# Optimization experiments

Hardware: AMD Instinct MI355X
Metric: run time of the kernel (lower is better)

The kernel has to match this reference:

```python
import jax, jax.numpy as jnp
import numpy as np

B, L, D, H = 2, 2048, 2048, 16
C = D // H  # head dim = 128
EPS = 1e-5


def setup_inputs() -> dict:
    key = jax.random.key(0)
    k1, k2, k3, k4 = jax.random.split(key, 4)
    scale = 1.0 / np.sqrt(D)
    return {
        "x": jax.random.normal(k1, (B, L, D), dtype=jnp.float32),
        "theta": jax.random.uniform(k2, (B, L, D // 2), dtype=jnp.float32) * 6.2831853,
        "w_qkv": jax.random.normal(k3, (3 * D, D), dtype=jnp.float32) * scale,
        "w_y": jax.random.normal(k4, (D, D), dtype=jnp.float32) * scale,
        "b_y": jnp.zeros((D,), dtype=jnp.float32),
    }


def _rms_norm(t):
    # RMSNorm over last dim, eps=1e-5, no affine
    return t * jax.lax.rsqrt(jnp.mean(t * t, axis=-1, keepdims=True) + EPS)


def _apply_rope(q, k, theta):
    # q, k: (B, H, L, C); theta: (B, H, L, C//2)
    qr, qi = q[..., 0::2], q[..., 1::2]
    kr, ki = k[..., 0::2], k[..., 1::2]
    cos_t, sin_t = jnp.cos(theta), jnp.sin(theta)
    q_rot = jnp.stack((qr * cos_t - qi * sin_t, qr * sin_t + qi * cos_t), axis=-1).reshape(q.shape)
    k_rot = jnp.stack((kr * cos_t - ki * sin_t, kr * sin_t + ki * cos_t), axis=-1).reshape(k.shape)
    return q_rot, k_rot


def reference(x, theta, w_qkv, w_y, b_y):
    # QKV projection: (B, L, 3D)
    qkv = jnp.einsum("bld,ed->ble", x, w_qkv)
    # rearrange '... L (n H C) -> n ... H L C'
    qkv = qkv.reshape(B, L, 3, H, C).transpose(2, 0, 3, 1, 4)  # (3, B, H, L, C)
    q, k, v = qkv[0], qkv[1], qkv[2]
    q, k = _rms_norm(q), _rms_norm(k)
    # theta: (B, L, H*C/2) -> (B, H, L, C/2)
    th = theta.reshape(B, L, H, C // 2).transpose(0, 2, 1, 3)
    q, k = _apply_rope(q, k, th)
    # scaled dot-product attention
    scores = jnp.einsum("bhqc,bhkc->bhqk", q, k) / np.sqrt(C).astype(np.float32)
    attn = jax.nn.softmax(scores, axis=-1)
    y = jnp.einsum("bhqk,bhkc->bhqc", attn, v)
    # (B, H, L, C) -> (B, L, H*C)
    y = y.transpose(0, 2, 1, 3).reshape(B, L, D)
    return jnp.einsum("bld,ed->ble", y, w_y) + b_y
```

## Files before the change

kernel.cpp:

```cpp
#include <hip/hip_runtime.h>
#include <stdint.h>

typedef uint16_t u16;
typedef __attribute__((ext_vector_type(8))) short bf16x8;
typedef __attribute__((ext_vector_type(4))) float f32x4;


__device__ __forceinline__ u16 f2bf(float f) {
  uint32_t u = __builtin_bit_cast(uint32_t, f);
  u += 0x7fffu + ((u >> 16) & 1u);
  return (u16)(u >> 16);
}
__device__ __forceinline__ float bf2f(u16 h) {
  return __builtin_bit_cast(float, (uint32_t)h << 16);
}
__device__ __forceinline__ uint32_t pack2bf(float a, float b) {
  uint32_t ua = __builtin_bit_cast(uint32_t, a) + 0x7fffu;
  uint32_t ub = __builtin_bit_cast(uint32_t, b) + 0x7fffu;
  return (ua >> 16) | (ub & 0xffff0000u);
}
__device__ __forceinline__ void gl_lds16(const u16* g, u16* l) {
  __builtin_amdgcn_global_load_lds((const __attribute__((address_space(1))) uint32_t*)g,
                                   (__attribute__((address_space(3))) uint32_t*)l, 16, 0, 0);
}

__global__ __launch_bounds__(256) void castk(const float* __restrict__ in,
                                             u16* __restrict__ out, int n) {
  int idx = (blockIdx.x * 256 + threadIdx.x) * 4;
  int stride = gridDim.x * 256 * 4;
  for (int i = idx; i < n; i += stride) {
    float4 v = *(const float4*)(in + i);
    uint32_t lo = (uint32_t)f2bf(v.x) | ((uint32_t)f2bf(v.y) << 16);
    uint32_t hi = (uint32_t)f2bf(v.z) | ((uint32_t)f2bf(v.w) << 16);
    *(uint2*)(out + i) = make_uint2(lo, hi);
  }
}

template <int MODE>
__global__ __launch_bounds__(256) void gemm_nt(
    const u16* __restrict__ A, const u16* __restrict__ Bw, int K,
    u16* __restrict__ qb, u16* __restrict__ kb, u16* __restrict__ vt,
    float* __restrict__ out, const float* __restrict__ bias) {
  __shared__ u16 As[128 * 64];
  __shared__ u16 Bs[128 * 64];
  const int tid = threadIdx.x;
  const int lane = tid & 63, wid = tid >> 6;
  const int g = lane >> 4, lr = lane & 15;
  const int wm = wid >> 1, wn = wid & 1;
  const int m0 = blockIdx.y * 128, n0 = blockIdx.x * 128;
  f32x4 acc[4][4] = {};
  const int nk = K >> 6;
  for (int kt = 0; kt < nk; ++kt) {
    const int kbase = kt * 64;
#pragma unroll
    for (int i = 0; i < 4; ++i) {
      int ci = wid * 256 + i * 64 + lane;
      int row = ci >> 3, j = ci & 7;
      int js = j ^ (row & 7);
      gl_lds16(A + (size_t)(m0 + row) * K + kbase + js * 8, &As[(wid * 256 + i * 64) * 8]);
    }
#pragma unroll
    for (int i = 0; i < 4; ++i) {
      int ci = wid * 256 + i * 64 + lane;
      int row = ci >> 3, j = ci & 7;
      int js = j ^ (row & 7);
      gl_lds16(Bw + (size_t)(n0 + row) * K + kbase + js * 8, &Bs[(wid * 256 + i * 64) * 8]);
    }
    __syncthreads();
#pragma unroll
    for (int ks = 0; ks < 2; ++ks) {
      bf16x8 af[4], bfr[4];
#pragma unroll
      for (int t = 0; t < 4; ++t) {
        int ra = wm * 64 + t * 16 + lr;
        af[t] = *(const bf16x8*)&As[ra * 64 + (((ks * 4 + g) ^ (ra & 7)) * 8)];
        int rb = wn * 64 + t * 16 + lr;
        bfr[t] = *(const bf16x8*)&Bs[rb * 64 + (((ks * 4 + g) ^ (rb & 7)) * 8)];
      }
#pragma unroll
      for (int mt = 0; mt < 4; ++mt)
#pragma unroll
        for (int nt = 0; nt < 4; ++nt)
          acc[mt][nt] =
              __builtin_amdgcn_mfma_f32_16x16x32_bf16(af[mt], bfr[nt], acc[mt][nt], 0, 0, 0);
    }
    __syncthreads();
  }
  if (MODE == 0) {
    const int s = n0 >> 11;
    const int h = (n0 >> 7) & 15;
#pragma unroll
    for (int mt = 0; mt < 4; ++mt)
#pragma unroll
      for (int nt = 0; nt < 4; ++nt) {
        int cblk = wn * 64 + nt * 16 + lr;
#pragma unroll
        for (int r = 0; r < 4; ++r) {
          int m = m0 + wm * 64 + mt * 16 + g * 4 + r;
          int b = m >> 11, lpos = m & 2047;
          u16 val = f2bf(acc[mt][nt][r]);
          if (s < 2) {
            u16* dst = (s == 0) ? qb : kb;
            dst[(size_t)((b * 16 + h) * 2048 + lpos) * 128 + cblk] = val;
          } else {
            vt[(size_t)((b * 16 + h) * 128 + cblk) * 2048 + lpos] = val;
          }
        }
      }
  } else {
#pragma unroll
    for (int mt = 0; mt < 4; ++mt)
#pragma unroll
      for (int nt = 0; nt < 4; ++nt) {
        int n = n0 + wn * 64 + nt * 16 + lr;
        float bv = bias[n];
#pragma unroll
        for (int r = 0; r < 4; ++r) {
          int m = m0 + wm * 64 + mt * 16 + g * 4 + r;
          out[(size_t)m * 2048 + n] = acc[mt][nt][r] + bv;
        }
      }
  }
}

__global__ __launch_bounds__(256) void qk_fix(u16* __restrict__ qb, u16* __restrict__ kb,
                                              const float* __restrict__ theta) {
  const int row = blockIdx.x * 4 + (threadIdx.x >> 6);
  const int lane = threadIdx.x & 63;
  const int bh = row >> 11, l = row & 2047;
  const int b = bh >> 4, h = bh & 15;
  float th = theta[(size_t)(b * 2048 + l) * 1024 + h * 64 + lane];
  float sn, cs;
  __sincosf(th, &sn, &cs);
#pragma unroll
  for (int which = 0; which < 2; ++which) {
    u16* buf = which ? kb : qb;
    uint32_t* p = (uint32_t*)(buf + (size_t)row * 128) + lane;
    uint32_t v = *p;
    float x0 = bf2f((u16)(v & 0xffff)), x1 = bf2f((u16)(v >> 16));
    float ss = x0 * x0 + x1 * x1;
#pragma unroll
    for (int m = 1; m <= 32; m <<= 1) ss += __shfl_xor(ss, m);
    float rn = rsqrtf(ss * (1.0f / 128.0f) + 1e-5f);
    if (which == 0) rn *= 0.12751743f;
    x0 *= rn;
    x1 *= rn;
    float y0 = x0 * cs - x1 * sn;
    float y1 = x0 * sn + x1 * cs;
    *p = (uint32_t)f2bf(y0) | ((uint32_t)f2bf(y1) << 16);
  }
}

__global__ __launch_bounds__(256, 2) void attn_k(const u16* __restrict__ qb,
                                                 const u16* __restrict__ kb,
                                                 const u16* __restrict__ vt,
                                                 u16* __restrict__ yb) {
  __shared__ u16 sm[32768];
  const int gid = blockIdx.x;
  const int slot = gid & 7, rest = gid >> 3;
  const int bh = slot * 4 + (rest & 3);
  const int qtile = rest >> 2;
  const int b = bh >> 4, h = bh & 15;
  const int tid = threadIdx.x, lane = tid & 63, wid = tid >> 6;
  const int g = lane >> 4, lr = lane & 15;
  const int q0 = qtile * 128 + wid * 32;

  bf16x8 qf[2][4];
#pragma unroll
  for (int qs = 0; qs < 2; ++qs) {
    const u16* qrow = qb + (size_t)(bh * 2048 + q0 + qs * 16 + lr) * 128;
#pragma unroll
    for (int ks = 0; ks < 4; ++ks) qf[qs][ks] = *(const bf16x8*)&qrow[ks * 32 + g * 8];
  }

  auto stage = [&](int buf, int kv) {
#pragma unroll
    for (int i = 0; i < 4; ++i) {
      int ci = i * 256 + tid;
      int row = ci >> 4, j = ci & 15;
      gl_lds16(kb + (size_t)(bh * 2048 + kv + row) * 128 + (j ^ (row & 7)) * 8,
               &sm[buf * 8192 + ci * 8]);
    }
#pragma unroll
    for (int i = 0; i < 4; ++i) {
      int ci = i * 256 + tid;
      int row = ci >> 3, j = ci & 7;
      gl_lds16(vt + (size_t)(bh * 128 + row) * 2048 + kv + (j ^ (row & 7)) * 8,
               &sm[16384 + buf * 8192 + ci * 8]);
    }
  };

  f32x4 acc[2][8] = {};
  float mrun[2] = {-1e30f, -1e30f}, lrun[2] = {0.f, 0.f};
  const int sA = (2 * (g & 1)) * 16 + lr, sB = sA + 16;
  const bool hi2 = (g >> 1) != 0;

  stage(0, 0);
  asm volatile("s_waitcnt vmcnt(0)" ::: "memory");
  __builtin_amdgcn_s_barrier();

  for (int t = 0; t < 32; ++t) {
    const int cur = t & 1;
    if (t < 31) stage(cur ^ 1, (t + 1) * 64);
    const u16* Ks = &sm[cur * 8192];
    const u16* Vs = &sm[16384 + cur * 8192];

    f32x4 st[2][4] = {};
#pragma unroll
    for (int ks = 0; ks < 4; ++ks) {
      bf16x8 kf[4];
#pragma unroll
      for (int kt = 0; kt < 4; ++kt) {
        int row = kt * 16 + lr;
        kf[kt] = *(const bf16x8*)&Ks[row * 128 + (((ks * 4 + g) ^ (row & 7)) * 8)];
      }
#pragma unroll
      for (int kt = 0; kt < 4; ++kt)
#pragma unroll
        for (int qs = 0; qs < 2; ++qs)
          st[qs][kt] =
              __builtin_amdgcn_mfma_f32_16x16x32_bf16(kf[kt], qf[qs][ks], st[qs][kt], 0, 0, 0);
    }

    float pmax[2];
#pragma unroll
    for (int qs = 0; qs < 2; ++qs) {
      float mx = st[qs][0][0];
#pragma unroll
      for (int kt = 0; kt < 4; ++kt)
#pragma unroll
        for (int r = 0; r < 4; ++r) mx = fmaxf(mx, st[qs][kt][r]);
      mx = fmaxf(mx, __shfl_xor(mx, 16));
      mx = fmaxf(mx, __shfl_xor(mx, 32));
      pmax[qs] = mx;
    }
    float need = fmaxf(pmax[0] - mrun[0], pmax[1] - mrun[1]);
    if (!__all(need <= 8.0f)) {
#pragma unroll
      for (int qs = 0; qs < 2; ++qs) {
        float mnew = fmaxf(mrun[qs], pmax[qs]);
        float corr = __builtin_amdgcn_exp2f(mrun[qs] - mnew);
        lrun[qs] *= corr;
        mrun[qs] = mnew;
#pragma unroll
        for (int ct = 0; ct < 8; ++ct) {
          acc[qs][ct][0] *= corr;
          acc[qs][ct][1] *= corr;
          acc[qs][ct][2] *= corr;
          acc[qs][ct][3] *= corr;
        }
      }
    }
    uint32_t pw[2][4][2];
#pragma unroll
    for (int qs = 0; qs < 2; ++qs) {
      float rsum = 0.f;
#pragma unroll
      for (int kt = 0; kt < 4; ++kt)
#pragma unroll
        for (int hf = 0; hf < 2; ++hf) {
          float e0 = __builtin_amdgcn_exp2f(st[qs][kt][2 * hf] - mrun[qs]);
          float e1 = __builtin_amdgcn_exp2f(st[qs][kt][2 * hf + 1] - mrun[qs]);
          rsum += e0 + e1;
          pw[qs][kt][hf] = pack2bf(e0, e1);
        }
      rsum += __shfl_xor(rsum, 16);
      rsum += __shfl_xor(rsum, 32);
      lrun[qs] += rsum;
    }

#pragma unroll
    for (int ks2 = 0; ks2 < 2; ++ks2) {
      bf16x8 pf[2];
#pragma unroll
      for (int qs = 0; qs < 2; ++qs) {
        uint32_t a0 = __shfl(pw[qs][ks2 * 2][0], sA);
        uint32_t a1 = __shfl(pw[qs][ks2 * 2][1], sA);
        uint32_t a2 = __shfl(pw[qs][ks2 * 2][0], sB);
        uint32_t a3 = __shfl(pw[qs][ks2 * 2][1], sB);
        uint32_t b0 = __shfl(pw[qs][ks2 * 2 + 1][0], sA);
        uint32_t b1 = __shfl(pw[qs][ks2 * 2 + 1][1], sA);
        uint32_t b2 = __shfl(pw[qs][ks2 * 2 + 1][0], sB);
        uint32_t b3 = __shfl(pw[qs][ks2 * 2 + 1][1], sB);
        union {
          uint32_t u[4];
          bf16x8 v;
        } tt;
        tt.u[0] = hi2 ? b0 : a0;
        tt.u[1] = hi2 ? b1 : a1;
        tt.u[2] = hi2 ? b2 : a2;
        tt.u[3] = hi2 ? b3 : a3;
        pf[qs] = tt.v;
      }
#pragma unroll
      for (int ct = 0; ct < 8; ++ct) {
        int row = ct * 16 + lr;
        bf16x8 vf = *(const bf16x8*)&Vs[row * 64 + (((ks2 * 4 + g) ^ (row & 7)) * 8)];
#pragma unroll
        for (int qs = 0; qs < 2; ++qs)
          acc[qs][ct] = __builtin_amdgcn_mfma_f32_16x16x32_bf16(vf, pf[qs], acc[qs][ct], 0, 0, 0);
      }
    }
    if (t < 31) {
      asm volatile("s_waitcnt vmcnt(0)" ::: "memory");
      __builtin_amdgcn_s_barrier();
    }
  }

#pragma unroll
  for (int qs = 0; qs < 2; ++qs) {
    float inv = 1.f / lrun[qs];
    const size_t orow = (size_t)(b * 2048 + q0 + qs * 16 + lr) * 2048 + h * 128;
#pragma unroll
    for (int ct = 0; ct < 8; ++ct) {
      uint32_t lo = pack2bf(acc[qs][ct][0] * inv, acc[qs][ct][1] * inv);
      uint32_t hi = pack2bf(acc[qs][ct][2] * inv, acc[qs][ct][3] * inv);
      *(uint2*)&yb[orow + ct * 16 + g * 4] = make_uint2(lo, hi);
    }
  }
}

extern "C" void kernel_launch(void* const* d_in, const int* in_sizes, int n_in,
                              void* d_out, int out_size, void* d_ws, size_t ws_size,
                              hipStream_t stream) {
  const float* x = (const float*)d_in[0];
  const float* theta = (const float*)d_in[1];
  const float* wqkv = (const float*)d_in[2];
  const float* wy = (const float*)d_in[3];
  const float* by = (const float*)d_in[4];
  float* out = (float*)d_out;
  char* ws = (char*)d_ws;
  u16* xb  = (u16*)(ws + 0);
  u16* wqb = (u16*)(ws + 16777216);
  u16* wyb = (u16*)(ws + 41943040);
  u16* qb  = (u16*)(ws + 50331648);
  u16* kb  = (u16*)(ws + 67108864);
  u16* vt  = (u16*)(ws + 83886080);
  u16* yb  = (u16*)(ws + 100663296);

  castk<<<2048, 256, 0, stream>>>(x, xb, 2 * 2048 * 2048);
  castk<<<2048, 256, 0, stream>>>(wqkv, wqb, 3 * 2048 * 2048);
  castk<<<1024, 256, 0, stream>>>(wy, wyb, 2048 * 2048);

  gemm_nt<0><<<dim3(48, 32), 256, 0, stream>>>(xb, wqb, 2048, qb, kb, vt, nullptr, nullptr);
  qk_fix<<<16384, 256, 0, stream>>>(qb, kb, theta);
  attn_k<<<512, 256, 0, stream>>>(qb, kb, vt, yb);
  gemm_nt<1><<<dim3(16, 32), 256, 0, stream>>>(yb, wyb, 2048, nullptr, nullptr, nullptr, out, by);
}
```

Baseline: 306.2 us.

## Replace QKV GEMM with 256x256-tile 8-wave double-buffered pipelined kernel

```diff
diff --git a/kernel.cpp b/kernel.cpp
--- a/kernel.cpp
+++ b/kernel.cpp
@@ -36,10 +36,112 @@
   }
 }
 
-template <int MODE>
-__global__ __launch_bounds__(256) void gemm_nt(
+__global__ __launch_bounds__(512, 2) void gemm8_qkv(
+    const u16* __restrict__ A, const u16* __restrict__ Bw,
+    u16* __restrict__ qb, u16* __restrict__ kb, u16* __restrict__ vt) {
+  __shared__ u16 sm[65536];
+  const int K = 2048;
+  const int tid = threadIdx.x, lane = tid & 63;
+  const int wid = tid >> 6, g = lane >> 4, lr = lane & 15;
+  const int wm = wid >> 2, wn = wid & 3;
+  const int m0 = blockIdx.y * 256, n0 = blockIdx.x * 256;
+  const int x7 = lr & 7;
+  const int srow = tid >> 3, sj = tid & 7, sjs = sj ^ (srow & 7);
+
+  auto stA = [&](int buf, int kt, int R) {
+    gl_lds16(A + (size_t)(m0 + R + srow) * K + kt * 64 + sjs * 8,
+             &sm[buf * 32768 + R * 64 + tid * 8]);
+  };
+  auto stB = [&](int buf, int kt, int R) {
+    gl_lds16(Bw + (size_t)(n0 + R + srow) * K + kt * 64 + sjs * 8,
+             &sm[buf * 32768 + 16384 + R * 64 + tid * 8]);
+  };
+
+  f32x4 acc[8][4] = {};
+
+  stB(0, 0, 0); stB(0, 0, 64); stB(0, 0, 128); stB(0, 0, 192);
+  stA(0, 0, 0); stA(0, 0, 128); stA(0, 0, 64); stA(0, 0, 192);
+  asm volatile("s_waitcnt vmcnt(2)" ::: "memory");
+  __builtin_amdgcn_s_barrier();
+
+  for (int t = 0; t < 32; ++t) {
+    const int cur = t & 1, nxt = cur ^ 1;
+    const int kn = (t < 31) ? t + 1 : 31;
+    const u16* As = &sm[cur * 32768];
+    const u16* Bs = &sm[cur * 32768 + 16384];
+    bf16x8 bfr[4][2];
+#pragma unroll
+    for (int p = 0; p < 4; ++p) {
+      bf16x8 af[2][2];
+#pragma unroll
+      for (int i = 0; i < 2; ++i)
+#pragma unroll
+        for (int ks = 0; ks < 2; ++ks)
+          af[i][ks] = *(const bf16x8*)&As[(wm * 128 + (p * 2 + i) * 16 + lr) * 64 +
+                                          (((ks * 4 + g) ^ x7) * 8)];
+      if (p == 0) {
+#pragma unroll
+        for (int nf = 0; nf < 4; ++nf)
+#pragma unroll
+          for (int ks = 0; ks < 2; ++ks)
+            bfr[nf][ks] = *(const bf16x8*)&Bs[(wn * 64 + nf * 16 + lr) * 64 +
+                                              (((ks * 4 + g) ^ x7) * 8)];
+        stB(nxt, kn, 0);
+        stB(nxt, kn, 64);
+      } else if (p == 1) {
+        stB(nxt, kn, 128);
+        stB(nxt, kn, 192);
+      } else if (p == 2) {
+        stA(nxt, kn, 0);
+        stA(nxt, kn, 128);
+      } else {
+        stA(nxt, kn, 64);
+        stA(nxt, kn, 192);
+      }
+      __builtin_amdgcn_s_barrier();
+      asm volatile("s_waitcnt lgkmcnt(0)" ::: "memory");
+      __builtin_amdgcn_sched_barrier(0);
+      __builtin_amdgcn_s_setprio(1);
+#pragma unroll
+      for (int i = 0; i < 2; ++i)
+#pragma unroll
+        for (int nf = 0; nf < 4; ++nf) {
+          acc[p * 2 + i][nf] = __builtin_amdgcn_mfma_f32_16x16x32_bf16(
+              af[i][0], bfr[nf][0], acc[p * 2 + i][nf], 0, 0, 0);
+          acc[p * 2 + i][nf] = __builtin_amdgcn_mfma_f32_16x16x32_bf16(
+              af[i][1], bfr[nf][1], acc[p * 2 + i][nf], 0, 0, 0);
+        }
+      __builtin_amdgcn_s_setprio(0);
+      if (p == 1) asm volatile("s_waitcnt vmcnt(4)" ::: "memory");
+      if (p == 3) asm volatile("s_waitcnt vmcnt(2)" ::: "memory");
+      __builtin_amdgcn_s_barrier();
+    }
+  }
+
+  const int s = n0 >> 11;
+#pragma unroll
+  for (int mf = 0; mf < 8; ++mf)
+#pragma unroll
+    for (int nf = 0; nf < 4; ++nf) {
+      int n = n0 + wn * 64 + nf * 16 + lr;
+      int h = (n >> 7) & 15, cb = n & 127;
+#pragma unroll
+      for (int r = 0; r < 4; ++r) {
+        int m = m0 + wm * 128 + mf * 16 + g * 4 + r;
+        int b = m >> 11, lp = m & 2047;
+        u16 val = f2bf(acc[mf][nf][r]);
+        if (s == 0)
+          qb[(size_t)((b * 16 + h) * 2048 + lp) * 128 + cb] = val;
+        else if (s == 1)
+          kb[(size_t)((b * 16 + h) * 2048 + lp) * 128 + cb] = val;
+        else
+          vt[(size_t)((b * 16 + h) * 128 + cb) * 2048 + lp] = val;
+      }
+    }
+}
+
+__global__ __launch_bounds__(256) void gemm_out(
     const u16* __restrict__ A, const u16* __restrict__ Bw, int K,
-    u16* __restrict__ qb, u16* __restrict__ kb, u16* __restrict__ vt,
     float* __restrict__ out, const float* __restrict__ bias) {
   __shared__ u16 As[128 * 64];
   __shared__ u16 Bs[128 * 64];
@@ -86,41 +188,18 @@
     }
     __syncthreads();
   }
-  if (MODE == 0) {
-    const int s = n0 >> 11;
-    const int h = (n0 >> 7) & 15;
-#pragma unroll
-    for (int mt = 0; mt < 4; ++mt)
-#pragma unroll
-      for (int nt = 0; nt < 4; ++nt) {
-        int cblk = wn * 64 + nt * 16 + lr;
-#pragma unroll
-        for (int r = 0; r < 4; ++r) {
-          int m = m0 + wm * 64 + mt * 16 + g * 4 + r;
-          int b = m >> 11, lpos = m & 2047;
-          u16 val = f2bf(acc[mt][nt][r]);
-          if (s < 2) {
-            u16* dst = (s == 0) ? qb : kb;
-            dst[(size_t)((b * 16 + h) * 2048 + lpos) * 128 + cblk] = val;
-          } else {
-            vt[(size_t)((b * 16 + h) * 128 + cblk) * 2048 + lpos] = val;
-          }
-        }
-      }
-  } else {
-#pragma unroll
-    for (int mt = 0; mt < 4; ++mt)
-#pragma unroll
-      for (int nt = 0; nt < 4; ++nt) {
-        int n = n0 + wn * 64 + nt * 16 + lr;
-        float bv = bias[n];
-#pragma unroll
-        for (int r = 0; r < 4; ++r) {
-          int m = m0 + wm * 64 + mt * 16 + g * 4 + r;
-          out[(size_t)m * 2048 + n] = acc[mt][nt][r] + bv;
-        }
-      }
-  }
+#pragma unroll
+  for (int mt = 0; mt < 4; ++mt)
+#pragma unroll
+    for (int nt = 0; nt < 4; ++nt) {
+      int n = n0 + wn * 64 + nt * 16 + lr;
+      float bv = bias[n];
+#pragma unroll
+      for (int r = 0; r < 4; ++r) {
+        int m = m0 + wm * 64 + mt * 16 + g * 4 + r;
+        out[(size_t)m * 2048 + n] = acc[mt][nt][r] + bv;
+      }
+    }
 }
 
 __global__ __launch_bounds__(256) void qk_fix(u16* __restrict__ qb, u16* __restrict__ kb,
@@ -342,8 +421,8 @@
   castk<<<2048, 256, 0, stream>>>(wqkv, wqb, 3 * 2048 * 2048);
   castk<<<1024, 256, 0, stream>>>(wy, wyb, 2048 * 2048);
 
-  gemm_nt<0><<<dim3(48, 32), 256, 0, stream>>>(xb, wqb, 2048, qb, kb, vt, nullptr, nullptr);
+  gemm8_qkv<<<dim3(24, 16), 512, 0, stream>>>(xb, wqb, qb, kb, vt);
   qk_fix<<<16384, 256, 0, stream>>>(qb, kb, theta);
   attn_k<<<512, 256, 0, stream>>>(qb, kb, vt, yb);
-  gemm_nt<1><<<dim3(16, 32), 256, 0, stream>>>(yb, wyb, 2048, nullptr, nullptr, nullptr, out, by);
-}
+  gemm_out<<<dim3(16, 32), 256, 0, stream>>>(yb, wyb, 2048, out, by);
+}
```

Measured after the change: 314.0 us. 2.5% more time.
